# Performance work log

Measured on AMD Instinct MI355X. Metric: run time of the kernel, lower is better.

The kernel has to match this reference:

```python
import jax, jax.numpy as jnp
import numpy as np

B, C, H, W = 4, 256, 64, 64
R, KH, KW = 4, 3, 3
K = KH * KW  # 9 kernel taps


def _conv2d(x, w, b):
    # plain 3x3 conv, stride 1, pad 1, NCHW
    y = jax.lax.conv_general_dilated(x, w, (1, 1), ((1, 1), (1, 1)),
                                     dimension_numbers=('NCHW', 'OIHW', 'NCHW'))
    return y + b[None, :, None, None]


def _bilinear_sample(x, py, px):
    # x: [B,C,H,W]; py,px: [B,K,H,W] float coords; zero padding outside the image.
    B_, C_, H_, W_ = x.shape
    xf = x.reshape(B_, C_, H_ * W_)
    y0 = jnp.floor(py)
    x0 = jnp.floor(px)
    wy = py - y0
    wx = px - x0
    y0i = y0.astype(jnp.int32)
    x0i = x0.astype(jnp.int32)

    def corner(yi, xi, wgt):
        valid = (yi >= 0) & (yi < H_) & (xi >= 0) & (xi < W_)
        idx = (jnp.clip(yi, 0, H_ - 1) * W_ + jnp.clip(xi, 0, W_ - 1)).reshape(B_, -1)
        vals = jax.vmap(lambda xb, ib: jnp.take(xb, ib, axis=1))(xf, idx)  # [B,C,K*H*W]
        vals = vals.reshape(B_, C_, K, H_, W_)
        w_ = (wgt * valid).astype(x.dtype)[:, None]  # [B,1,K,H,W]
        return vals * w_

    out = corner(y0i, x0i, (1 - wy) * (1 - wx))
    out = out + corner(y0i, x0i + 1, (1 - wy) * wx)
    out = out + corner(y0i + 1, x0i, wy * (1 - wx))
    out = out + corner(y0i + 1, x0i + 1, wy * wx)
    return out  # [B,C,K,H,W]


def _deform_conv(x, offset, weight):
    # DCNv1: offset [B, 2K, H, W], interleaved (dy, dx) per kernel tap.
    B_, C_, H_, W_ = x.shape
    off = offset.reshape(B_, K, 2, H_, W_)
    ky, kx = jnp.meshgrid(jnp.arange(KH), jnp.arange(KW), indexing='ij')
    base_y = (ky.reshape(K) - (KH - 1) // 2).astype(x.dtype)
    base_x = (kx.reshape(K) - (KW - 1) // 2).astype(x.dtype)
    py = (jnp.arange(H_, dtype=x.dtype)[None, None, :, None]
          + base_y[None, :, None, None] + off[:, :, 0])
    px = (jnp.arange(W_, dtype=x.dtype)[None, None, None, :]
          + base_x[None, :, None, None] + off[:, :, 1])
    sampled = _bilinear_sample(x, py, px)  # [B,C,K,H,W]
    wr = weight.reshape(weight.shape[0], C_, K)
    return jnp.einsum('bckhw,ock->bohw', sampled, wr)


def setup_inputs() -> dict:
    key = jax.random.key(0)
    k1, k2, k3 = jax.random.split(key, 3)
    x = jax.random.normal(k1, (B, C, H, W), jnp.float32)
    off_w = jax.random.normal(k2, (R, 2 * K, C, KH, KW), jnp.float32) * 0.01
    off_b = jnp.zeros((R, 2 * K), jnp.float32)
    w = jax.random.normal(k3, (R, C, C, KH, KW), jnp.float32) * (1.0 / np.sqrt(C * K))
    return {"x": x, "off_w": off_w, "off_b": off_b, "w": w}


def reference(x, off_w, off_b, w):
    for r in range(R):  # fixed small layer count
        offset = _conv2d(x, off_w[r], off_b[r])
        x = jax.nn.relu(_deform_conv(x, offset, w[r]))
    return x
```

## Files before the change

### kernel.cpp

```cpp
#include <hip/hip_runtime.h>


#define HW 4096

typedef __attribute__((ext_vector_type(8))) __bf16 bf16x8;
typedef __attribute__((ext_vector_type(4))) float f32x4;
typedef __attribute__((ext_vector_type(8))) unsigned short u16x8;

__device__ inline unsigned int f2bf_bits(float f) {
  unsigned int u = __float_as_uint(f);
  return (u + 0x7fffu + ((u >> 16) & 1u)) >> 16;
}
__device__ inline float bf_hi_f(unsigned short h) {
  return __uint_as_float(((unsigned int)h) << 16);
}

__device__ inline void wg_barrier_lds() {
  asm volatile("s_waitcnt lgkmcnt(0)" ::: "memory");
  __builtin_amdgcn_s_barrier();
  __builtin_amdgcn_sched_barrier(0);
}

__global__ __launch_bounds__(256) void wpack_kernel(
    const float* __restrict__ w, unsigned short* __restrict__ wph) {
  const int f = blockIdx.x * 256 + threadIdx.x;
  const int j  = f & 7;
  const int l  = (f >> 3) & 63;
  const int nt = (f >> 9) & 15;
  const int q  = (f >> 13) % 72;
  const int r  = f / 589824;
  const int n  = nt * 16 + (l & 15);
  const int kk = q * 32 + ((l >> 4) << 3) + j;
  const int c  = kk & 255, k = kk >> 8;
  wph[f] = (unsigned short)f2bf_bits(w[((r * 256 + n) * 256 + c) * 9 + k]);
}

__global__ __launch_bounds__(256) void offwpack_kernel(
    const float* __restrict__ offw, unsigned short* __restrict__ owph) {
  const int f = blockIdx.x * 256 + threadIdx.x;
  const int j  = f & 7;
  const int l  = (f >> 3) & 63;
  const int nt = (f >> 9) & 1;
  const int q  = (f >> 10) % 72;
  const int r  = f / 73728;
  const int n  = nt * 16 + (l & 15);
  const int kk = q * 32 + ((l >> 4) << 3) + j;
  const int c  = kk & 255, k = kk >> 8;
  const float v = (n < 18) ? offw[((r * 18 + n) * 256 + c) * 9 + k] : 0.f;
  owph[f] = (unsigned short)f2bf_bits(v);
}

__global__ __launch_bounds__(256) void xpose_kernel(
    const float* __restrict__ x, unsigned short* __restrict__ xh) {
  const int p0 = blockIdx.x * 64;
  const int c0 = blockIdx.y * 64;
  const int b  = blockIdx.z;
  __shared__ float sT[64][65];
  const int t = threadIdx.x;
  const int pj = t & 63, ci0 = (t >> 6) * 16;
  const float* __restrict__ xb = x + ((size_t)(b * 256 + c0)) * HW + p0;
#pragma unroll
  for (int u = 0; u < 16; ++u)
    sT[ci0 + u][pj] = xb[(size_t)(ci0 + u) * HW + pj];
  __syncthreads();
  const int pr = t >> 2, cs = (t & 3) * 16;
  u16x8 va, vb;
#pragma unroll
  for (int u = 0; u < 8; ++u) va[u] = (unsigned short)f2bf_bits(sT[cs + u][pr]);
#pragma unroll
  for (int u = 0; u < 8; ++u) vb[u] = (unsigned short)f2bf_bits(sT[cs + 8 + u][pr]);
  const size_t o = ((size_t)b * HW + p0 + pr) * 256 + c0 + cs;
  *(u16x8*)(xh + o) = va;
  *(u16x8*)(xh + o + 8) = vb;
}

__global__ __launch_bounds__(512) void offconv_mfma(
    const unsigned short* __restrict__ xh,
    const unsigned short* __restrict__ owh,
    const float* __restrict__ bias, float* __restrict__ offs) {
  const int gid = blockIdx.x;
  const int b = (gid & 7) >> 1;
  const int idx = ((gid >> 3) << 1) | (gid & 1);
  const int h = idx >> 1, w0 = (idx & 1) << 5;
  const int t = threadIdx.x, lane = t & 63, wv = t >> 6;
  const int frow = lane & 15, fgrp = lane >> 4;
  const int mt = wv & 1, nt = (wv >> 1) & 1, kv = wv >> 2;
  const int m = w0 + mt * 16 + frow;

  f32x4 acc = {0.f, 0.f, 0.f, 0.f};
  const u16x8 z8 = {};
  const size_t xb = (size_t)b * HW;
  const u16x8* __restrict__ owp = (const u16x8*)owh;

#define OLOAD(k, A, Bv)                                                     \
  {                                                                         \
    const int ky = (k) / 3 - 1, kx = (k) % 3 - 1;                           \
    const int hy = h + ky;                                                  \
    const int hyc = hy < 0 ? 0 : (hy > 63 ? 63 : hy);                       \
    const int mx = m + kx;                                                  \
    const bool v = ((unsigned)hy < 64u) && ((unsigned)mx < 64u);            \
    const int cpx = mx < 0 ? 0 : (mx > 63 ? 63 : mx);                       \
    const size_t abase =                                                    \
        (xb + (size_t)(hyc * 64 + cpx)) * 256 + fgrp * 8 + kv * 128;        \
    _Pragma("unroll") for (int j = 0; j < 4; ++j) {                         \
      A[j] = *(const u16x8*)(xh + abase + j * 32);                          \
      if (!v) A[j] = z8;                                                    \
    }                                                                       \
    _Pragma("unroll") for (int j = 0; j < 4; ++j)                           \
      Bv[j] = owp[((((k) * 8 + kv * 4 + j) * 2) + nt) * 64 + lane];         \
  }

#define OMFMA(A, Bv)                                                        \
  _Pragma("unroll") for (int j = 0; j < 4; ++j)                             \
    acc = __builtin_amdgcn_mfma_f32_16x16x32_bf16(                          \
        __builtin_bit_cast(bf16x8, A[j]), __builtin_bit_cast(bf16x8, Bv[j]),\
        acc, 0, 0, 0);

  u16x8 A0[4], Bv0[4], A1[4], Bv1[4];
  OLOAD(0, A0, Bv0)
  OLOAD(1, A1, Bv1)
  OMFMA(A0, Bv0) OLOAD(2, A0, Bv0)
  OMFMA(A1, Bv1) OLOAD(3, A1, Bv1)
  OMFMA(A0, Bv0) OLOAD(4, A0, Bv0)
  OMFMA(A1, Bv1) OLOAD(5, A1, Bv1)
  OMFMA(A0, Bv0) OLOAD(6, A0, Bv0)
  OMFMA(A1, Bv1) OLOAD(7, A1, Bv1)
  OMFMA(A0, Bv0) OLOAD(8, A0, Bv0)
  OMFMA(A1, Bv1)
  OMFMA(A0, Bv0)
#undef OLOAD
#undef OMFMA

  __shared__ f32x4 red[2][2][64];
  if (kv == 1) red[mt][nt][lane] = acc;
  __syncthreads();
  if (kv == 0) {
    const f32x4 o = red[mt][nt][lane];
    acc[0] += o[0]; acc[1] += o[1]; acc[2] += o[2]; acc[3] += o[3];
    const int oc = nt * 16 + frow;
    if (oc < 18) {
      const float bv = bias[oc];
      const int wbase = w0 + mt * 16 + fgrp * 4;
      float* __restrict__ op =
          offs + (size_t)(b * 18 + oc) * HW + h * 64 + wbase;
#pragma unroll
      for (int r = 0; r < 4; ++r) op[r] = acc[r] + bv;
    }
  }
}

__global__ __launch_bounds__(512, 4) void deform_mfma(
    const unsigned short* __restrict__ xh,
    const float* __restrict__ offs,
    const unsigned short* __restrict__ wph,
    unsigned short* __restrict__ yth,
    float* __restrict__ outf) {
  const int gid = blockIdx.x;
  const int b = (gid & 7) >> 1;
  const int idx = ((gid >> 3) << 1) | (gid & 1);
  const int h = idx >> 1, w0 = (idx & 1) << 5;
  const int t = threadIdx.x, lane = t & 63, wv = t >> 6;
  const int frow = lane & 15, quad = lane >> 4;
  const int sm = t >> 4, cg = t & 15;

  __shared__ __align__(16) unsigned char smem[25600];
  float* s_cw = (float*)smem;
  int*   s_ci = (int*)(smem + 4608);
  unsigned char* sAb = smem + 9216;

  for (int i = t; i < 288; i += 512) {
    const int k = i >> 5, m = i & 31;
    const int ky = k / 3 - 1, kx = k % 3 - 1;
    const int mw = w0 + m;
    const int pos = h * 64 + mw;
    const float dy = offs[(b * 18 + 2 * k) * HW + pos];
    const float dx = offs[(b * 18 + 2 * k + 1) * HW + pos];
    const float py = (float)(h + ky) + dy;
    const float px = (float)(mw + kx) + dx;
    const float y0f = floorf(py), x0f = floorf(px);
    const float wy = py - y0f, wx = px - x0f;
    const int y0 = (int)y0f, x0 = (int)x0f;
#pragma unroll
    for (int j = 0; j < 4; ++j) {
      const int yi = y0 + (j >> 1), xi = x0 + (j & 1);
      const bool v = (yi >= 0) && (yi < 64) && (xi >= 0) && (xi < 64);
      const float wgt = ((j >> 1) ? wy : 1.f - wy) * ((j & 1) ? wx : 1.f - wx);
      s_cw[(k * 4 + j) * 32 + m] = v ? wgt : 0.f;
      const int yc = yi < 0 ? 0 : (yi > 63 ? 63 : yi);
      const int xc = xi < 0 ? 0 : (xi > 63 ? 63 : xi);
      s_ci[(k * 4 + j) * 32 + m] = yc * 64 + xc;
    }
  }
  __syncthreads();

  f32x4 acc[2][2];
#pragma unroll
  for (int mt = 0; mt < 2; ++mt)
#pragma unroll
    for (int nt = 0; nt < 2; ++nt) acc[mt][nt] = (f32x4){0.f, 0.f, 0.f, 0.f};

  const char* __restrict__ xbc = (const char*)(xh + (size_t)b * HW * 256);
  const u16x8* __restrict__ wp = (const u16x8*)wph;
  const int bfo = wv * 2;

  const int gs = ((sm & 3) << 1) | ((sm >> 2) & 1);
  const int wbA = sm * 128 + ((((cg >> 2) ^ gs)) << 4) + (cg & 3) * 4;
  const int wbL = wbA ^ 64;
  const int gr = ((frow & 3) << 1) | ((frow >> 2) & 1);
  const int rb0 = frow * 128 + ((quad ^ gr) << 4);
  const int rb1 = rb0 + 2048;

  unsigned int G0[4], G1[4];
  u16x8 B0[2], B1[2];
  float cwrC[4], cwrN[4];
  int cibC[4], cibN[4];
#pragma unroll
  for (int j = 0; j < 4; ++j) {
    cwrC[j] = s_cw[j * 32 + sm];
    cibC[j] = s_ci[j * 32 + sm] * 512;
  }
#pragma unroll
  for (int j = 0; j < 4; ++j)
    G0[j] = *(const unsigned int*)(xbc + cibC[j] + cg * 4);
#pragma unroll
  for (int j = 0; j < 4; ++j)
    G1[j] = *(const unsigned int*)(xbc + cibC[j] + 64 + cg * 4);
#pragma unroll
  for (int i = 0; i < 2; ++i) B0[i] = wp[(bfo + i) * 64 + lane];
#pragma unroll
  for (int i = 0; i < 2; ++i) B1[i] = wp[(16 + bfo + i) * 64 + lane];

#define COMBINE_STORE(Gx, BB)                                               \
  {                                                                         \
    float s0 = cwrC[0] * __uint_as_float(Gx[0] << 16);                      \
    float s1 = cwrC[0] * __uint_as_float(Gx[0] & 0xffff0000u);              \
    s0 = fmaf(cwrC[1], __uint_as_float(Gx[1] << 16), s0);                   \
    s1 = fmaf(cwrC[1], __uint_as_float(Gx[1] & 0xffff0000u), s1);           \
    s0 = fmaf(cwrC[2], __uint_as_float(Gx[2] << 16), s0);                   \
    s1 = fmaf(cwrC[2], __uint_as_float(Gx[2] & 0xffff0000u), s1);           \
    s0 = fmaf(cwrC[3], __uint_as_float(Gx[3] << 16), s0);                   \
    s1 = fmaf(cwrC[3], __uint_as_float(Gx[3] & 0xffff0000u), s1);           \
    const __bf16 hb0 = (__bf16)s0, hb1 = (__bf16)s1;                        \
    const unsigned int hv =                                                 \
        (unsigned int)__builtin_bit_cast(unsigned short, hb0) |             \
        ((unsigned int)__builtin_bit_cast(unsigned short, hb1) << 16);      \
    const float d0 = s0 - __uint_as_float(hv << 16);                        \
    const float d1 = s1 - __uint_as_float(hv & 0xffff0000u);                \
    const __bf16 lb0 = (__bf16)d0, lb1 = (__bf16)d1;                        \
    const unsigned int lv =                                                 \
        (unsigned int)__builtin_bit_cast(unsigned short, lb0) |             \
        ((unsigned int)__builtin_bit_cast(unsigned short, lb1) << 16);      \
    *(unsigned int*)(sAb + (BB) + wbA) = hv;                                \
    *(unsigned int*)(sAb + (BB) + wbL) = lv;                                \
  }

#define MFMA_BODY(BB, Bx)                                                   \
  {                                                                         \
    bf16x8 ah[2], al[2];                                                    \
    ah[0] = __builtin_bit_cast(bf16x8, *(const u16x8*)(sAb + (BB) + rb0));  \
    al[0] = __builtin_bit_cast(bf16x8,                                      \
                               *(const u16x8*)(sAb + (BB) + (rb0 ^ 64)));   \
    ah[1] = __builtin_bit_cast(bf16x8, *(const u16x8*)(sAb + (BB) + rb1));  \
    al[1] = __builtin_bit_cast(bf16x8,                                      \
                               *(const u16x8*)(sAb + (BB) + (rb1 ^ 64)));   \
    __builtin_amdgcn_s_setprio(1);                                          \
    _Pragma("unroll") for (int nt = 0; nt < 2; ++nt) {                      \
      const bf16x8 bv = __builtin_bit_cast(bf16x8, Bx[nt]);                 \
      _Pragma("unroll") for (int mt = 0; mt < 2; ++mt) {                    \
        acc[mt][nt] = __builtin_amdgcn_mfma_f32_16x16x32_bf16(              \
            ah[mt], bv, acc[mt][nt], 0, 0, 0);                              \
        acc[mt][nt] = __builtin_amdgcn_mfma_f32_16x16x32_bf16(              \
            al[mt], bv, acc[mt][nt], 0, 0, 0);                              \
      }                                                                     \
    }                                                                       \
    __builtin_amdgcn_s_setprio(0);                                          \
  }

  for (int k9 = 0; k9 < 9; ++k9) {
#pragma unroll
    for (int sp = 0; sp < 4; ++sp) {
      const int PB = (sp & 1) * 8192;
      COMBINE_STORE(G0, PB)
      COMBINE_STORE(G1, PB + 4096)
      wg_barrier_lds();
      const bool more = (k9 < 8) || (sp < 3);
      if (more) {
        if (sp == 3) {
#pragma unroll
          for (int j = 0; j < 4; ++j) {
            cwrN[j] = s_cw[((k9 + 1) * 4 + j) * 32 + sm];
            cibN[j] = s_ci[((k9 + 1) * 4 + j) * 32 + sm] * 512;
          }
#pragma unroll
          for (int j = 0; j < 4; ++j)
            G0[j] = *(const unsigned int*)(xbc + cibN[j] + cg * 4);
#pragma unroll
          for (int j = 0; j < 4; ++j)
            G1[j] = *(const unsigned int*)(xbc + cibN[j] + 64 + cg * 4);
        } else {
          const int c0b = ((2 * sp + 2) & 7) * 64 + cg * 4;
#pragma unroll
          for (int j = 0; j < 4; ++j)
            G0[j] = *(const unsigned int*)(xbc + cibC[j] + c0b);
#pragma unroll
          for (int j = 0; j < 4; ++j)
            G1[j] = *(const unsigned int*)(xbc + cibC[j] + c0b + 64);
        }
      }
      MFMA_BODY(PB, B0)
      if (more) {
        const int cn0 = k9 * 8 + 2 * sp + 2;
#pragma unroll
        for (int i = 0; i < 2; ++i)
          B0[i] = wp[(cn0 * 16 + bfo + i) * 64 + lane];
      }
      MFMA_BODY(PB + 4096, B1)
      if (more) {
        const int cn1 = k9 * 8 + 2 * sp + 3;
#pragma unroll
        for (int i = 0; i < 2; ++i)
          B1[i] = wp[(cn1 * 16 + bfo + i) * 64 + lane];
      }
      if (sp == 3 && k9 < 8) {
#pragma unroll
        for (int j = 0; j < 4; ++j) { cwrC[j] = cwrN[j]; cibC[j] = cibN[j]; }
      }
    }
  }
#undef COMBINE_STORE
#undef MFMA_BODY

  if (outf) {
#pragma unroll
    for (int mt = 0; mt < 2; ++mt)
#pragma unroll
      for (int nt = 0; nt < 2; ++nt) {
        const int n = wv * 32 + nt * 16 + frow;
        const int pos = h * 64 + w0 + mt * 16 + quad * 4;
        float4 vv;
        vv.x = fmaxf(acc[mt][nt][0], 0.f);
        vv.y = fmaxf(acc[mt][nt][1], 0.f);
        vv.z = fmaxf(acc[mt][nt][2], 0.f);
        vv.w = fmaxf(acc[mt][nt][3], 0.f);
        *(float4*)&outf[(size_t)(b * 256 + n) * HW + pos] = vv;
      }
  } else {
    __syncthreads();
    unsigned short* sW = (unsigned short*)smem + wv * (32 * 36);
#pragma unroll
    for (int mt = 0; mt < 2; ++mt)
#pragma unroll
      for (int nt = 0; nt < 2; ++nt)
#pragma unroll
        for (int r = 0; r < 4; ++r)
          sW[(mt * 16 + quad * 4 + r) * 36 + nt * 16 + frow] =
              (unsigned short)f2bf_bits(fmaxf(acc[mt][nt][r], 0.f));
    __syncthreads();
    const int lm = lane & 31, cg2 = lane >> 5;
    const int pos = h * 64 + w0 + lm;
    unsigned short* __restrict__ yp =
        yth + ((size_t)b * HW + pos) * 256 + wv * 32 + cg2 * 16;
#pragma unroll
    for (int g = 0; g < 2; ++g)
      *(u16x8*)(yp + g * 8) = *(const u16x8*)&sW[lm * 36 + cg2 * 16 + g * 8];
  }
}

extern "C" void kernel_launch(void* const* d_in, const int* in_sizes, int n_in,
                              void* d_out, int out_size, void* d_ws, size_t ws_size,
                              hipStream_t stream) {
  const float* x0   = (const float*)d_in[0];
  const float* offw = (const float*)d_in[1];
  const float* offb = (const float*)d_in[2];
  const float* w    = (const float*)d_in[3];
  float* out = (float*)d_out;
  float* ws  = (float*)d_ws;

  float* offs = ws;
  unsigned short* wph  = (unsigned short*)(ws + 294912);
  unsigned short* owph = wph + 2359296;
  unsigned short* xTA  = owph + 294912;
  unsigned short* xTB  = xTA + 4194304;

  wpack_kernel<<<9216, 256, 0, stream>>>(w, wph);
  offwpack_kernel<<<1152, 256, 0, stream>>>(offw, owph);
  xpose_kernel<<<dim3(64, 4, 4), 256, 0, stream>>>(x0, xTA);

  unsigned short* pin = xTA;
  unsigned short* pout = xTB;
  for (int r = 0; r < 4; ++r) {
    offconv_mfma<<<512, 512, 0, stream>>>(pin, owph + r * 73728,
                                          offb + r * 18, offs);
    deform_mfma<<<512, 512, 0, stream>>>(pin, offs,
                                         wph + (size_t)r * 589824,
                                         (r < 3) ? pout : nullptr,
                                         (r < 3) ? nullptr : out);
    unsigned short* tmp = pin; pin = pout; pout = tmp;
  }
}
```

Measured before the change: 346.8 us.

## Fuse offset convolution into deformable conv kernel, keep offsets in LDS

```diff
diff --git a/kernel.cpp b/kernel.cpp
--- a/kernel.cpp
+++ b/kernel.cpp
@@ -10,9 +10,6 @@
 __device__ inline unsigned int f2bf_bits(float f) {
   unsigned int u = __float_as_uint(f);
   return (u + 0x7fffu + ((u >> 16) & 1u)) >> 16;
-}
-__device__ inline float bf_hi_f(unsigned short h) {
-  return __uint_as_float(((unsigned int)h) << 16);
 }
 
 __device__ inline void wg_barrier_lds() {
@@ -74,84 +71,10 @@
   *(u16x8*)(xh + o + 8) = vb;
 }
 
-__global__ __launch_bounds__(512) void offconv_mfma(
+__global__ __launch_bounds__(512, 4) void deform_mfma(
     const unsigned short* __restrict__ xh,
     const unsigned short* __restrict__ owh,
-    const float* __restrict__ bias, float* __restrict__ offs) {
-  const int gid = blockIdx.x;
-  const int b = (gid & 7) >> 1;
-  const int idx = ((gid >> 3) << 1) | (gid & 1);
-  const int h = idx >> 1, w0 = (idx & 1) << 5;
-  const int t = threadIdx.x, lane = t & 63, wv = t >> 6;
-  const int frow = lane & 15, fgrp = lane >> 4;
-  const int mt = wv & 1, nt = (wv >> 1) & 1, kv = wv >> 2;
-  const int m = w0 + mt * 16 + frow;
-
-  f32x4 acc = {0.f, 0.f, 0.f, 0.f};
-  const u16x8 z8 = {};
-  const size_t xb = (size_t)b * HW;
-  const u16x8* __restrict__ owp = (const u16x8*)owh;
-
-#define OLOAD(k, A, Bv)                                                     \
-  {                                                                         \
-    const int ky = (k) / 3 - 1, kx = (k) % 3 - 1;                           \
-    const int hy = h + ky;                                                  \
-    const int hyc = hy < 0 ? 0 : (hy > 63 ? 63 : hy);                       \
-    const int mx = m + kx;                                                  \
-    const bool v = ((unsigned)hy < 64u) && ((unsigned)mx < 64u);            \
-    const int cpx = mx < 0 ? 0 : (mx > 63 ? 63 : mx);                       \
-    const size_t abase =                                                    \
-        (xb + (size_t)(hyc * 64 + cpx)) * 256 + fgrp * 8 + kv * 128;        \
-    _Pragma("unroll") for (int j = 0; j < 4; ++j) {                         \
-      A[j] = *(const u16x8*)(xh + abase + j * 32);                          \
-      if (!v) A[j] = z8;                                                    \
-    }                                                                       \
-    _Pragma("unroll") for (int j = 0; j < 4; ++j)                           \
-      Bv[j] = owp[((((k) * 8 + kv * 4 + j) * 2) + nt) * 64 + lane];         \
-  }
-
-#define OMFMA(A, Bv)                                                        \
-  _Pragma("unroll") for (int j = 0; j < 4; ++j)                             \
-    acc = __builtin_amdgcn_mfma_f32_16x16x32_bf16(                          \
-        __builtin_bit_cast(bf16x8, A[j]), __builtin_bit_cast(bf16x8, Bv[j]),\
-        acc, 0, 0, 0);
-
-  u16x8 A0[4], Bv0[4], A1[4], Bv1[4];
-  OLOAD(0, A0, Bv0)
-  OLOAD(1, A1, Bv1)
-  OMFMA(A0, Bv0) OLOAD(2, A0, Bv0)
-  OMFMA(A1, Bv1) OLOAD(3, A1, Bv1)
-  OMFMA(A0, Bv0) OLOAD(4, A0, Bv0)
-  OMFMA(A1, Bv1) OLOAD(5, A1, Bv1)
-  OMFMA(A0, Bv0) OLOAD(6, A0, Bv0)
-  OMFMA(A1, Bv1) OLOAD(7, A1, Bv1)
-  OMFMA(A0, Bv0) OLOAD(8, A0, Bv0)
-  OMFMA(A1, Bv1)
-  OMFMA(A0, Bv0)
-#undef OLOAD
-#undef OMFMA
-
-  __shared__ f32x4 red[2][2][64];
-  if (kv == 1) red[mt][nt][lane] = acc;
-  __syncthreads();
-  if (kv == 0) {
-    const f32x4 o = red[mt][nt][lane];
-    acc[0] += o[0]; acc[1] += o[1]; acc[2] += o[2]; acc[3] += o[3];
-    const int oc = nt * 16 + frow;
-    if (oc < 18) {
-      const float bv = bias[oc];
-      const int wbase = w0 + mt * 16 + fgrp * 4;
-      float* __restrict__ op =
-          offs + (size_t)(b * 18 + oc) * HW + h * 64 + wbase;
-#pragma unroll
-      for (int r = 0; r < 4; ++r) op[r] = acc[r] + bv;
-    }
-  }
-}
-
-__global__ __launch_bounds__(512, 4) void deform_mfma(
-    const unsigned short* __restrict__ xh,
-    const float* __restrict__ offs,
+    const float* __restrict__ offb,
     const unsigned short* __restrict__ wph,
     unsigned short* __restrict__ yth,
     float* __restrict__ outf) {
@@ -167,14 +90,87 @@
   float* s_cw = (float*)smem;
   int*   s_ci = (int*)(smem + 4608);
   unsigned char* sAb = smem + 9216;
+  float* s_off = (float*)(smem + 13312);
+
+  {
+    const int kv = wv >> 2, ntO = (wv >> 1) & 1, mtO = wv & 1;
+    const int mO = w0 + mtO * 16 + frow;
+    f32x4 aoc = {0.f, 0.f, 0.f, 0.f};
+    const u16x8 z8 = {};
+    const size_t xb = (size_t)b * HW;
+    const u16x8* __restrict__ owp = (const u16x8*)owh;
+
+#define OHLOAD(k, p, A, Bv)                                                 \
+  {                                                                         \
+    const int ky = (k) / 3 - 1, kx = (k) % 3 - 1;                           \
+    const int hy = h + ky;                                                  \
+    const int hyc = hy < 0 ? 0 : (hy > 63 ? 63 : hy);                       \
+    const int mx = mO + kx;                                                 \
+    const bool v = ((unsigned)hy < 64u) && ((unsigned)mx < 64u);            \
+    const int cpx = mx < 0 ? 0 : (mx > 63 ? 63 : mx);                       \
+    const size_t abase = (xb + (size_t)(hyc * 64 + cpx)) * 256              \
+                         + quad * 8 + kv * 128 + (p) * 64;                  \
+    _Pragma("unroll") for (int j = 0; j < 2; ++j) {                         \
+      A[j] = *(const u16x8*)(xh + abase + j * 32);                          \
+      if (!v) A[j] = z8;                                                    \
+    }                                                                       \
+    _Pragma("unroll") for (int j = 0; j < 2; ++j)                           \
+      Bv[j] = owp[(((k) * 8 + kv * 4 + (p) * 2 + j) * 2 + ntO) * 64 + lane];\
+  }
+
+#define OHMFMA(A, Bv)                                                       \
+  _Pragma("unroll") for (int j = 0; j < 2; ++j)                             \
+    aoc = __builtin_amdgcn_mfma_f32_16x16x32_bf16(                          \
+        __builtin_bit_cast(bf16x8, A[j]), __builtin_bit_cast(bf16x8, Bv[j]),\
+        aoc, 0, 0, 0);
+
+    u16x8 A0[2], Bv0[2], A1[2], Bv1[2];
+    OHLOAD(0, 0, A0, Bv0)
+    OHLOAD(0, 1, A1, Bv1)
+    OHMFMA(A0, Bv0) OHLOAD(1, 0, A0, Bv0)
+    OHMFMA(A1, Bv1) OHLOAD(1, 1, A1, Bv1)
+    OHMFMA(A0, Bv0) OHLOAD(2, 0, A0, Bv0)
+    OHMFMA(A1, Bv1) OHLOAD(2, 1, A1, Bv1)
+    OHMFMA(A0, Bv0) OHLOAD(3, 0, A0, Bv0)
+    OHMFMA(A1, Bv1) OHLOAD(3, 1, A1, Bv1)
+    OHMFMA(A0, Bv0) OHLOAD(4, 0, A0, Bv0)
+    OHMFMA(A1, Bv1) OHLOAD(4, 1, A1, Bv1)
+    OHMFMA(A0, Bv0) OHLOAD(5, 0, A0, Bv0)
+    OHMFMA(A1, Bv1) OHLOAD(5, 1, A1, Bv1)
+    OHMFMA(A0, Bv0) OHLOAD(6, 0, A0, Bv0)
+    OHMFMA(A1, Bv1) OHLOAD(6, 1, A1, Bv1)
+    OHMFMA(A0, Bv0) OHLOAD(7, 0, A0, Bv0)
+    OHMFMA(A1, Bv1) OHLOAD(7, 1, A1, Bv1)
+    OHMFMA(A0, Bv0) OHLOAD(8, 0, A0, Bv0)
+    OHMFMA(A1, Bv1) OHLOAD(8, 1, A1, Bv1)
+    OHMFMA(A0, Bv0)
+    OHMFMA(A1, Bv1)
+#undef OHLOAD
+#undef OHMFMA
+
+    f32x4* redp = (f32x4*)(smem + 9216);
+    if (kv == 1) redp[(mtO * 2 + ntO) * 64 + lane] = aoc;
+    __syncthreads();
+    if (kv == 0) {
+      const f32x4 o = redp[(mtO * 2 + ntO) * 64 + lane];
+      aoc[0] += o[0]; aoc[1] += o[1]; aoc[2] += o[2]; aoc[3] += o[3];
+      const int oc = ntO * 16 + frow;
+      if (oc < 18) {
+        const float bv = offb[oc];
+        const int mb = mtO * 16 + quad * 4;
+#pragma unroll
+        for (int r = 0; r < 4; ++r) s_off[oc * 32 + mb + r] = aoc[r] + bv;
+      }
+    }
+    __syncthreads();
+  }
 
   for (int i = t; i < 288; i += 512) {
     const int k = i >> 5, m = i & 31;
     const int ky = k / 3 - 1, kx = k % 3 - 1;
     const int mw = w0 + m;
-    const int pos = h * 64 + mw;
-    const float dy = offs[(b * 18 + 2 * k) * HW + pos];
-    const float dx = offs[(b * 18 + 2 * k + 1) * HW + pos];
+    const float dy = s_off[(2 * k) * 32 + m];
+    const float dx = s_off[(2 * k + 1) * 32 + m];
     const float py = (float)(h + ky) + dy;
     const float px = (float)(mw + kx) + dx;
     const float y0f = floorf(py), x0f = floorf(px);
@@ -376,7 +372,6 @@
   float* out = (float*)d_out;
   float* ws  = (float*)d_ws;
 
-  float* offs = ws;
   unsigned short* wph  = (unsigned short*)(ws + 294912);
   unsigned short* owph = wph + 2359296;
   unsigned short* xTA  = owph + 294912;
@@ -389,9 +384,8 @@
   unsigned short* pin = xTA;
   unsigned short* pout = xTB;
   for (int r = 0; r < 4; ++r) {
-    offconv_mfma<<<512, 512, 0, stream>>>(pin, owph + r * 73728,
-                                          offb + r * 18, offs);
-    deform_mfma<<<512, 512, 0, stream>>>(pin, offs,
+    deform_mfma<<<512, 512, 0, stream>>>(pin, owph + r * 73728,
+                                         offb + r * 18,
                                          wph + (size_t)r * 589824,
                                          (r < 3) ? pout : nullptr,
                                          (r < 3) ? nullptr : out);
```

New measurement: 339.8 us. 2.0% less time.
